# Kernel optimization log

Hardware: AMD Instinct MI355X
Metric: run time of the kernel (lower is better)

## Reference

```python
import jax, jax.numpy as jnp
import numpy as np

B, S, D, H, O, E, TOPK = 4, 2048, 512, 1024, 512, 8, 2


def setup_inputs() -> dict:
    key = jax.random.key(0)
    ks = jax.random.split(key, 6)
    s = lambda d: 1.0 / np.sqrt(d)
    return {
        "x": jax.random.normal(ks[0], (B, S, D), dtype=jnp.float32),
        "Wg": jax.random.normal(ks[1], (D, E), dtype=jnp.float32) * s(D),
        "W1": jax.random.normal(ks[2], (E, D, H), dtype=jnp.float32) * s(D),
        "b1": jnp.zeros((E, H), dtype=jnp.float32),
        "W2": jax.random.normal(ks[3], (E, H, O), dtype=jnp.float32) * s(H),
        "b2": jnp.zeros((E, O), dtype=jnp.float32),
    }


def reference(x, Wg, W1, b1, W2, b2):
    Bsz, Seq, Din = x.shape
    T = Bsz * Seq
    xm = x.reshape(T, Din)                       # [T, D] token matrix
    # router: softmax over experts, then top-k (ProbabilitySamplerTopk)
    probs = jax.nn.softmax(xm @ Wg, axis=-1)     # [T, E]
    top_p, top_i = jax.lax.top_k(probs, TOPK)    # [T, k]
    # dense scattered gates (topKProbabilitiesScattered in _computeGating);
    # zero entries for non-selected experts make the einsum combine exactly
    # equal to the original gather->per-expert-GEMM->index_add pipeline.
    gates = jnp.zeros((T, E), dtype=probs.dtype).at[
        jnp.arange(T)[:, None], top_i
    ].set(top_p)                                 # [T, E]
    # per-expert 2-layer MLP (inputExperts -> activation -> outputExperts)
    h = jax.nn.gelu(jnp.einsum("td,edh->teh", xm, W1) + b1[None])  # [T, E, H]
    y = jnp.einsum("teh,eho->teo", h, W2) + b2[None]               # [T, E, O]
    # weighted combine (multiply_by_gates + index_add)
    out = jnp.einsum("te,teo->to", gates, y)     # [T, O]
    return out.reshape(Bsz, Seq, O)
```

## Files before the change

### kernel.cpp

```cpp
#include <hip/hip_runtime.h>

#define T_TOK 8192
#define DIM   512
#define HID   1024
#define OUTD  512
#define NE    8

typedef __attribute__((ext_vector_type(8))) short short8v;
typedef __attribute__((ext_vector_type(4))) float f32x4;

__device__ __forceinline__ unsigned short f2bf(float f) {
  unsigned int u = __builtin_bit_cast(unsigned int, f);
  u += 0x7fffu + ((u >> 16) & 1u);
  return (unsigned short)(u >> 16);
}

__device__ __forceinline__ void gload_lds16(const void* g, void* l) {
  __builtin_amdgcn_global_load_lds(
      (__attribute__((address_space(1))) void*)g,
      (__attribute__((address_space(3))) void*)l, 16, 0, 0);
}

__device__ __forceinline__ float gelu_f(float v) {
  const float c0 = 0.7978845608028654f;
  float u = c0 * (v + 0.044715f * v * v * v);
  return 0.5f * v * (1.0f + tanhf(u));
}

__global__ __launch_bounds__(256) void k_transpose_cvt(
    const float* __restrict__ in, unsigned short* __restrict__ outp, int R, int C) {
  __shared__ float tile[32][33];
  int e = blockIdx.z;
  const float* inE = in + (size_t)e * R * C;
  unsigned short* outE = outp + (size_t)e * R * C;
  int c0 = blockIdx.x * 32, r0 = blockIdx.y * 32;
  int x = threadIdx.x, y = threadIdx.y;
#pragma unroll
  for (int i = 0; i < 32; i += 8)
    tile[y + i][x] = inE[(size_t)(r0 + y + i) * C + (c0 + x)];
  __syncthreads();
#pragma unroll
  for (int i = 0; i < 32; i += 8)
    outE[(size_t)(c0 + y + i) * R + (r0 + x)] = f2bf(tile[x][y + i]);
}

__global__ __launch_bounds__(256) void k_router(
    const float* __restrict__ x, const float* __restrict__ Wg,
    int* __restrict__ top_e, float* __restrict__ top_p) {
  int lane = threadIdx.x & 63;
  int t = blockIdx.x * 4 + (threadIdx.x >> 6);
  const float* xr = x + (size_t)t * DIM;
  int j0 = lane * 8;
  float4 xa = *(const float4*)(xr + j0);
  float4 xb = *(const float4*)(xr + j0 + 4);
  float xl[8] = {xa.x, xa.y, xa.z, xa.w, xb.x, xb.y, xb.z, xb.w};
  float acc[8] = {0.f,0.f,0.f,0.f,0.f,0.f,0.f,0.f};
#pragma unroll
  for (int jj = 0; jj < 8; ++jj) {
    float4 w0 = *(const float4*)(Wg + (size_t)(j0 + jj) * NE);
    float4 w1 = *(const float4*)(Wg + (size_t)(j0 + jj) * NE + 4);
    acc[0] += xl[jj] * w0.x; acc[1] += xl[jj] * w0.y;
    acc[2] += xl[jj] * w0.z; acc[3] += xl[jj] * w0.w;
    acc[4] += xl[jj] * w1.x; acc[5] += xl[jj] * w1.y;
    acc[6] += xl[jj] * w1.z; acc[7] += xl[jj] * w1.w;
  }
#pragma unroll
  for (int off = 32; off >= 1; off >>= 1) {
#pragma unroll
    for (int e2 = 0; e2 < 8; ++e2) acc[e2] += __shfl_xor(acc[e2], off, 64);
  }
  if (lane == 0) {
    float m = acc[0];
#pragma unroll
    for (int e2 = 1; e2 < 8; ++e2) m = fmaxf(m, acc[e2]);
    float p[8]; float s = 0.f;
#pragma unroll
    for (int e2 = 0; e2 < 8; ++e2) { p[e2] = expf(acc[e2] - m); s += p[e2]; }
    float inv = 1.f / s;
    int i0 = 0;
#pragma unroll
    for (int e2 = 1; e2 < 8; ++e2) if (p[e2] > p[i0]) i0 = e2;
    int i1 = (i0 == 0) ? 1 : 0;
#pragma unroll
    for (int e2 = 0; e2 < 8; ++e2) if (e2 != i0 && p[e2] > p[i1]) i1 = e2;
    top_e[t * 2] = i0;  top_e[t * 2 + 1] = i1;
    top_p[t * 2] = p[i0] * inv;  top_p[t * 2 + 1] = p[i1] * inv;
  }
}

__global__ __launch_bounds__(256) void k_plan(
    const int* __restrict__ top_e, int* __restrict__ localRank,
    int* __restrict__ blockCounts) {
  __shared__ int cnt[4][NE];
  __shared__ int wbase[4][NE];
  int tid = threadIdx.x, lane = tid & 63, w = tid >> 6;
  int a = blockIdx.x * 256 + tid;
  int e = top_e[a];
  int rank = 0;
#pragma unroll
  for (int e2 = 0; e2 < NE; ++e2) {
    unsigned long long m = __ballot(e == e2);
    if (e == e2) rank = __popcll(m & ((1ULL << lane) - 1ULL));
    if (lane == 0) cnt[w][e2] = __popcll(m);
  }
  __syncthreads();
  if (tid < NE) {
    int s = 0;
#pragma unroll
    for (int w2 = 0; w2 < 4; ++w2) { wbase[w2][tid] = s; s += cnt[w2][tid]; }
    blockCounts[blockIdx.x * NE + tid] = s;
  }
  __syncthreads();
  localRank[a] = wbase[w][e] + rank;
}

__global__ void k_scan2(const int* __restrict__ blockCounts, int* __restrict__ baseBlk,
                        int* __restrict__ offs, int nBlocks) {
  __shared__ int tot[NE];
  int tid = threadIdx.x;
  if (tid < NE) {
    int s = 0;
    for (int b = 0; b < nBlocks; ++b) { baseBlk[b * NE + tid] = s; s += blockCounts[b * NE + tid]; }
    tot[tid] = s;
  }
  __syncthreads();
  if (tid == 0) {
    int s = 0;
    for (int e = 0; e < NE; ++e) { offs[e] = s; s += tot[e]; }
    offs[NE] = s;
  }
}

__global__ __launch_bounds__(256) void k_scatter(
    const float* __restrict__ x, const int* __restrict__ top_e,
    const int* __restrict__ localRank, const int* __restrict__ baseBlk,
    const int* __restrict__ offs, int* __restrict__ pos_of,
    unsigned short* __restrict__ Xp) {
  int lane = threadIdx.x & 63;
  int a = blockIdx.x * 4 + (threadIdx.x >> 6);
  int t = a >> 1;
  int e = top_e[a];
  int pos = offs[e] + baseBlk[(a >> 8) * NE + e] + localRank[a];
  if (lane == 0) pos_of[a] = pos;
  const float* xr = x + (size_t)t * DIM + lane * 8;
  float4 xa = *(const float4*)xr;
  float4 xb = *(const float4*)(xr + 4);
  short8v pk;
  pk[0] = (short)f2bf(xa.x); pk[1] = (short)f2bf(xa.y);
  pk[2] = (short)f2bf(xa.z); pk[3] = (short)f2bf(xa.w);
  pk[4] = (short)f2bf(xb.x); pk[5] = (short)f2bf(xb.y);
  pk[6] = (short)f2bf(xb.z); pk[7] = (short)f2bf(xb.w);
  *(short8v*)(Xp + (size_t)pos * DIM + lane * 8) = pk;
}

#define MFMA1(d, a, b) d = __builtin_amdgcn_mfma_f32_16x16x32_bf16(a, b, d, 0, 0, 0)

template<int NX, int LOG2NX, int EPI>
__global__ __launch_bounds__(256, 4) void k_gemm_x(
    const unsigned short* __restrict__ A,
    const unsigned short* __restrict__ Bt,
    const float* __restrict__ bias,
    const int* __restrict__ offs,
    unsigned short* __restrict__ Hout, float* __restrict__ Yout, int K, int N) {
  __shared__ __align__(16) unsigned short Al[128 * 64];
  __shared__ __align__(16) unsigned short Bl[128 * 64];

  const int e = blockIdx.x & 7;
  const int slot = blockIdx.x >> 3;
  const int nSlots = gridDim.x >> 3;
  const int rowBeg = offs[e], rowEnd = offs[e + 1];
  if (rowBeg >= rowEnd) return;
  const int nMT = (rowEnd - rowBeg + 127) >> 7;
  const int nWork = nMT << LOG2NX;
  const unsigned short* Be = Bt + (size_t)e * N * K;

  const int tid = threadIdx.x, lane = tid & 63, w = tid >> 6;
  const int wr = w >> 1, wc = w & 1;
  const int fr = lane & 15, fq = lane >> 4;
  const int sRow = tid >> 3;
  const int sCe = ((((tid & 7) << 4) ^ ((sRow & 7) << 4)) >> 1);
  const int NT = K >> 6;

  for (int idx = slot; idx < nWork; idx += nSlots) {
    const int mt = idx >> LOG2NX;
    const int xb = idx & (NX - 1);
    const int m0 = rowBeg + mt * 128;
    const int n0 = xb * 128;

    f32x4 acc[4][4];
#pragma unroll
    for (int m = 0; m < 4; ++m)
#pragma unroll
      for (int n = 0; n < 4; ++n) acc[m][n] = (f32x4){0.f, 0.f, 0.f, 0.f};

    for (int t = 0; t < NT; ++t) {
#pragma unroll
      for (int c_ = 0; c_ < 4; ++c_) {
        int ar_ = m0 + c_ * 32 + sRow; if (ar_ > rowEnd - 1) ar_ = rowEnd - 1;
        gload_lds16(A + (size_t)ar_ * K + (t << 6) + sCe,
                    (char*)&Al[0] + c_ * 4096 + (w << 10));
      }
#pragma unroll
      for (int c_ = 0; c_ < 4; ++c_) {
        int br_ = n0 + c_ * 32 + sRow;
        gload_lds16(Be + (size_t)br_ * K + (t << 6) + sCe,
                    (char*)&Bl[0] + c_ * 4096 + (w << 10));
      }
      __syncthreads();
#pragma unroll
      for (int kk = 0; kk < 2; ++kk) {
        short8v av[4], bv[4];
#pragma unroll
        for (int m = 0; m < 4; ++m) {
          int row_ = wr * 64 + m * 16 + fr;
          av[m] = *(const short8v*)((const char*)&Al[0] + row_ * 128 +
                    (((kk << 6) + (fq << 4)) ^ ((fr & 7) << 4)));
        }
#pragma unroll
        for (int n = 0; n < 4; ++n) {
          int row_ = wc * 64 + n * 16 + fr;
          bv[n] = *(const short8v*)((const char*)&Bl[0] + row_ * 128 +
                    (((kk << 6) + (fq << 4)) ^ ((fr & 7) << 4)));
        }
#pragma unroll
        for (int m = 0; m < 4; ++m)
#pragma unroll
          for (int n = 0; n < 4; ++n)
            MFMA1(acc[m][n], av[m], bv[n]);
      }
      __syncthreads();
    }

#pragma unroll
    for (int m = 0; m < 4; ++m) {
#pragma unroll
      for (int j = 0; j < 4; ++j) {
        int row = m0 + wr * 64 + m * 16 + fq * 4 + j;
        if (row >= rowEnd) continue;
#pragma unroll
        for (int n = 0; n < 4; ++n) {
          int col = n0 + wc * 64 + n * 16 + fr;
          float v = acc[m][n][j] + bias[(size_t)e * N + col];
          if (EPI == 0) Hout[(size_t)row * N + col] = f2bf(gelu_f(v));
          else          Yout[(size_t)row * N + col] = v;
        }
      }
    }
  }
}

__global__ __launch_bounds__(256) void k_combine(
    const float* __restrict__ Y, const int* __restrict__ pos_of,
    const float* __restrict__ top_p, float* __restrict__ out) {
  int lane = threadIdx.x & 63;
  int t = blockIdx.x * 4 + (threadIdx.x >> 6);
  int p0 = pos_of[t * 2], p1 = pos_of[t * 2 + 1];
  float g0 = top_p[t * 2], g1 = top_p[t * 2 + 1];
  const float4* y0 = (const float4*)(Y + (size_t)p0 * OUTD + lane * 8);
  const float4* y1 = (const float4*)(Y + (size_t)p1 * OUTD + lane * 8);
  float4* o = (float4*)(out + (size_t)t * OUTD + lane * 8);
  float4 a0 = y0[0], a1 = y0[1], c0 = y1[0], c1 = y1[1];
  float4 r0, r1;
  r0.x = g0 * a0.x + g1 * c0.x; r0.y = g0 * a0.y + g1 * c0.y;
  r0.z = g0 * a0.z + g1 * c0.z; r0.w = g0 * a0.w + g1 * c0.w;
  r1.x = g0 * a1.x + g1 * c1.x; r1.y = g0 * a1.y + g1 * c1.y;
  r1.z = g0 * a1.z + g1 * c1.z; r1.w = g0 * a1.w + g1 * c1.w;
  o[0] = r0; o[1] = r1;
}

extern "C" void kernel_launch(void* const* d_in, const int* in_sizes, int n_in,
                              void* d_out, int out_size, void* d_ws, size_t ws_size,
                              hipStream_t stream) {
  const float* x  = (const float*)d_in[0];
  const float* Wg = (const float*)d_in[1];
  const float* W1 = (const float*)d_in[2];
  const float* b1 = (const float*)d_in[3];
  const float* W2 = (const float*)d_in[4];
  const float* b2 = (const float*)d_in[5];
  float* out = (float*)d_out;

  char* p = (char*)d_ws;
  auto take = [&](size_t bytes) { char* r = p; p += (bytes + 255) & ~(size_t)255; return r; };
  unsigned short* W1t = (unsigned short*)take((size_t)NE * DIM * HID * 2);
  unsigned short* W2t = (unsigned short*)take((size_t)NE * HID * OUTD * 2);
  unsigned short* Xp  = (unsigned short*)take((size_t)2 * T_TOK * DIM * 2);
  unsigned short* Hb  = (unsigned short*)take((size_t)2 * T_TOK * HID * 2);
  float*          Yb  = (float*)take((size_t)2 * T_TOK * OUTD * 4);
  int* offs   = (int*)take(4096);
  int*   top_e  = (int*)take((size_t)2 * T_TOK * 4);
  float* top_pv = (float*)take((size_t)2 * T_TOK * 4);
  int*   pos_of = (int*)take((size_t)2 * T_TOK * 4);
  int* localRank   = (int*)take((size_t)2 * T_TOK * 4);
  int* blockCounts = (int*)take((size_t)64 * NE * 4);
  int* baseBlk     = (int*)take((size_t)64 * NE * 4);

  const int PLAN_BLOCKS = (2 * T_TOK) / 256;

  k_transpose_cvt<<<dim3(HID / 32, DIM / 32, NE), dim3(32, 8), 0, stream>>>(W1, W1t, DIM, HID);
  k_transpose_cvt<<<dim3(OUTD / 32, HID / 32, NE), dim3(32, 8), 0, stream>>>(W2, W2t, HID, OUTD);
  k_router<<<T_TOK / 4, 256, 0, stream>>>(x, Wg, top_e, top_pv);
  k_plan<<<PLAN_BLOCKS, 256, 0, stream>>>(top_e, localRank, blockCounts);
  k_scan2<<<1, 64, 0, stream>>>(blockCounts, baseBlk, offs, PLAN_BLOCKS);
  k_scatter<<<(2 * T_TOK) / 4, 256, 0, stream>>>(x, top_e, localRank, baseBlk, offs, pos_of, Xp);
  k_gemm_x<8, 3, 0><<<1024, 256, 0, stream>>>(Xp, W1t, b1, offs, Hb, nullptr, DIM, HID);
  k_gemm_x<4, 2, 1><<<512, 256, 0, stream>>>(Hb, W2t, b2, offs, nullptr, Yb, HID, OUTD);
  k_combine<<<T_TOK / 4, 256, 0, stream>>>(Yb, pos_of, top_pv, out);
}
```

Measured before the change: 153.5 us.

## Store second GEMM output as bf16, merge weight transposes, cheaper GELU

Several independent changes. The second expert GEMM now writes its output as bf16 instead of fp32, halving the intermediate write and the combine kernel's reads. The two weight transpose/convert launches are merged into one kernel, and GELU's tanhf is replaced by an equivalent exp-based sigmoid form using __expf. The GEMM's per-iteration address arithmetic is hoisted into precomputed row pointers. The bf16 intermediate adds rounding error before the gated combine.

New measurement: 132.8 us. -13.5%, faster.

```diff
diff --git a/kernel.cpp b/kernel.cpp
--- a/kernel.cpp
+++ b/kernel.cpp
@@ -15,6 +15,11 @@
   return (unsigned short)(u >> 16);
 }
 
+__device__ __forceinline__ float bf2f(unsigned short h) {
+  unsigned int u = ((unsigned int)h) << 16;
+  return __builtin_bit_cast(float, u);
+}
+
 __device__ __forceinline__ void gload_lds16(const void* g, void* l) {
   __builtin_amdgcn_global_load_lds(
       (__attribute__((address_space(1))) void*)g,
@@ -24,16 +29,26 @@
 __device__ __forceinline__ float gelu_f(float v) {
   const float c0 = 0.7978845608028654f;
   float u = c0 * (v + 0.044715f * v * v * v);
-  return 0.5f * v * (1.0f + tanhf(u));
-}
-
-__global__ __launch_bounds__(256) void k_transpose_cvt(
-    const float* __restrict__ in, unsigned short* __restrict__ outp, int R, int C) {
+  return v / (1.0f + __expf(-2.0f * u));
+}
+
+__global__ __launch_bounds__(256) void k_trans_all(
+    const float* __restrict__ W1, const float* __restrict__ W2,
+    unsigned short* __restrict__ W1t, unsigned short* __restrict__ W2t) {
   __shared__ float tile[32][33];
-  int e = blockIdx.z;
-  const float* inE = in + (size_t)e * R * C;
-  unsigned short* outE = outp + (size_t)e * R * C;
-  int c0 = blockIdx.x * 32, r0 = blockIdx.y * 32;
+  int bid = blockIdx.x;
+  int which = bid >> 12;
+  int r = bid & 4095;
+  int e = r >> 9;
+  int t = r & 511;
+  int R = which ? HID : DIM;
+  int C = which ? OUTD : HID;
+  int tx, ty;
+  if (which == 0) { ty = t >> 5; tx = t & 31; }
+  else            { ty = t >> 4; tx = t & 15; }
+  const float* inE = (which ? W2 : W1) + (size_t)e * R * C;
+  unsigned short* outE = (which ? W2t : W1t) + (size_t)e * R * C;
+  int c0 = tx * 32, r0 = ty * 32;
   int x = threadIdx.x, y = threadIdx.y;
 #pragma unroll
   for (int i = 0; i < 32; i += 8)
@@ -161,7 +176,8 @@
     const unsigned short* __restrict__ Bt,
     const float* __restrict__ bias,
     const int* __restrict__ offs,
-    unsigned short* __restrict__ Hout, float* __restrict__ Yout, int K, int N) {
+    unsigned short* __restrict__ Hout, unsigned short* __restrict__ Ybf,
+    int K, int N) {
   __shared__ __align__(16) unsigned short Al[128 * 64];
   __shared__ __align__(16) unsigned short Bl[128 * 64];
 
@@ -187,6 +203,15 @@
     const int m0 = rowBeg + mt * 128;
     const int n0 = xb * 128;
 
+    const char* aP[4]; const char* bP[4];
+#pragma unroll
+    for (int c_ = 0; c_ < 4; ++c_) {
+      int ar_ = m0 + c_ * 32 + sRow; if (ar_ > rowEnd - 1) ar_ = rowEnd - 1;
+      aP[c_] = (const char*)(A + (size_t)ar_ * K + sCe);
+      int br_ = n0 + c_ * 32 + sRow;
+      bP[c_] = (const char*)(Be + (size_t)br_ * K + sCe);
+    }
+
     f32x4 acc[4][4];
 #pragma unroll
     for (int m = 0; m < 4; ++m)
@@ -194,18 +219,13 @@
       for (int n = 0; n < 4; ++n) acc[m][n] = (f32x4){0.f, 0.f, 0.f, 0.f};
 
     for (int t = 0; t < NT; ++t) {
-#pragma unroll
-      for (int c_ = 0; c_ < 4; ++c_) {
-        int ar_ = m0 + c_ * 32 + sRow; if (ar_ > rowEnd - 1) ar_ = rowEnd - 1;
-        gload_lds16(A + (size_t)ar_ * K + (t << 6) + sCe,
-                    (char*)&Al[0] + c_ * 4096 + (w << 10));
-      }
-#pragma unroll
-      for (int c_ = 0; c_ < 4; ++c_) {
-        int br_ = n0 + c_ * 32 + sRow;
-        gload_lds16(Be + (size_t)br_ * K + (t << 6) + sCe,
-                    (char*)&Bl[0] + c_ * 4096 + (w << 10));
-      }
+      const int tOff = t << 7;
+#pragma unroll
+      for (int c_ = 0; c_ < 4; ++c_)
+        gload_lds16(aP[c_] + tOff, (char*)&Al[0] + c_ * 4096 + (w << 10));
+#pragma unroll
+      for (int c_ = 0; c_ < 4; ++c_)
+        gload_lds16(bP[c_] + tOff, (char*)&Bl[0] + c_ * 4096 + (w << 10));
       __syncthreads();
 #pragma unroll
       for (int kk = 0; kk < 2; ++kk) {
@@ -242,7 +262,7 @@
           int col = n0 + wc * 64 + n * 16 + fr;
           float v = acc[m][n][j] + bias[(size_t)e * N + col];
           if (EPI == 0) Hout[(size_t)row * N + col] = f2bf(gelu_f(v));
-          else          Yout[(size_t)row * N + col] = v;
+          else          Ybf[(size_t)row * N + col] = f2bf(v);
         }
       }
     }
@@ -250,21 +270,24 @@
 }
 
 __global__ __launch_bounds__(256) void k_combine(
-    const float* __restrict__ Y, const int* __restrict__ pos_of,
+    const unsigned short* __restrict__ Y, const int* __restrict__ pos_of,
     const float* __restrict__ top_p, float* __restrict__ out) {
   int lane = threadIdx.x & 63;
   int t = blockIdx.x * 4 + (threadIdx.x >> 6);
   int p0 = pos_of[t * 2], p1 = pos_of[t * 2 + 1];
   float g0 = top_p[t * 2], g1 = top_p[t * 2 + 1];
-  const float4* y0 = (const float4*)(Y + (size_t)p0 * OUTD + lane * 8);
-  const float4* y1 = (const float4*)(Y + (size_t)p1 * OUTD + lane * 8);
+  short8v ya = *(const short8v*)(Y + (size_t)p0 * OUTD + lane * 8);
+  short8v yb = *(const short8v*)(Y + (size_t)p1 * OUTD + lane * 8);
+  float4 r0, r1;
+  r0.x = g0 * bf2f((unsigned short)ya[0]) + g1 * bf2f((unsigned short)yb[0]);
+  r0.y = g0 * bf2f((unsigned short)ya[1]) + g1 * bf2f((unsigned short)yb[1]);
+  r0.z = g0 * bf2f((unsigned short)ya[2]) + g1 * bf2f((unsigned short)yb[2]);
+  r0.w = g0 * bf2f((unsigned short)ya[3]) + g1 * bf2f((unsigned short)yb[3]);
+  r1.x = g0 * bf2f((unsigned short)ya[4]) + g1 * bf2f((unsigned short)yb[4]);
+  r1.y = g0 * bf2f((unsigned short)ya[5]) + g1 * bf2f((unsigned short)yb[5]);
+  r1.z = g0 * bf2f((unsigned short)ya[6]) + g1 * bf2f((unsigned short)yb[6]);
+  r1.w = g0 * bf2f((unsigned short)ya[7]) + g1 * bf2f((unsigned short)yb[7]);
   float4* o = (float4*)(out + (size_t)t * OUTD + lane * 8);
-  float4 a0 = y0[0], a1 = y0[1], c0 = y1[0], c1 = y1[1];
-  float4 r0, r1;
-  r0.x = g0 * a0.x + g1 * c0.x; r0.y = g0 * a0.y + g1 * c0.y;
-  r0.z = g0 * a0.z + g1 * c0.z; r0.w = g0 * a0.w + g1 * c0.w;
-  r1.x = g0 * a1.x + g1 * c1.x; r1.y = g0 * a1.y + g1 * c1.y;
-  r1.z = g0 * a1.z + g1 * c1.z; r1.w = g0 * a1.w + g1 * c1.w;
   o[0] = r0; o[1] = r1;
 }
 
@@ -285,7 +308,7 @@
   unsigned short* W2t = (unsigned short*)take((size_t)NE * HID * OUTD * 2);
   unsigned short* Xp  = (unsigned short*)take((size_t)2 * T_TOK * DIM * 2);
   unsigned short* Hb  = (unsigned short*)take((size_t)2 * T_TOK * HID * 2);
-  float*          Yb  = (float*)take((size_t)2 * T_TOK * OUTD * 4);
+  unsigned short* Yb  = (unsigned short*)take((size_t)2 * T_TOK * OUTD * 2);
   int* offs   = (int*)take(4096);
   int*   top_e  = (int*)take((size_t)2 * T_TOK * 4);
   float* top_pv = (float*)take((size_t)2 * T_TOK * 4);
@@ -296,8 +319,7 @@
 
   const int PLAN_BLOCKS = (2 * T_TOK) / 256;
 
-  k_transpose_cvt<<<dim3(HID / 32, DIM / 32, NE), dim3(32, 8), 0, stream>>>(W1, W1t, DIM, HID);
-  k_transpose_cvt<<<dim3(OUTD / 32, HID / 32, NE), dim3(32, 8), 0, stream>>>(W2, W2t, HID, OUTD);
+  k_trans_all<<<8192, dim3(32, 8), 0, stream>>>(W1, W2, W1t, W2t);
   k_router<<<T_TOK / 4, 256, 0, stream>>>(x, Wg, top_e, top_pv);
   k_plan<<<PLAN_BLOCKS, 256, 0, stream>>>(top_e, localRank, blockCounts);
   k_scan2<<<1, 64, 0, stream>>>(blockCounts, baseBlk, offs, PLAN_BLOCKS);
```
